# Performance work log

Hardware: AMD Instinct MI355X
Metric: run time of the kernel (lower is better)

## Reference

```python
import jax, jax.numpy as jnp
import numpy as np

B, T, D, S = 32, 4096, 64, 64
H = 128  # emission MLP hidden width
EPS = 1e-10
NEG = 1e10


def setup_inputs() -> dict:
    key = jax.random.key(0)
    ks = jax.random.split(key, 8)

    def dense_init(k, shape):
        return jax.random.normal(k, shape, jnp.float32) / jnp.sqrt(shape[0])

    return {
        "observations": jax.random.normal(ks[0], (B, T, D), jnp.float32),
        "W1": dense_init(ks[1], (D, H)), "b1": jnp.zeros((H,), jnp.float32),
        "W2": dense_init(ks[2], (H, H)), "b2": jnp.zeros((H,), jnp.float32),
        "W3": dense_init(ks[3], (H, S)), "b3": jnp.zeros((S,), jnp.float32),
        "log_trans_matrix": jax.random.normal(ks[4], (S, S), jnp.float32) * 0.1,
        "log_init_probs": jnp.zeros((S,), jnp.float32),
        "log_r": jnp.ones((S,), jnp.float32),
        "logit_p": jnp.zeros((S,), jnp.float32),
    }


def reference(observations, W1, b1, W2, b2, W3, b3,
              log_trans_matrix, log_init_probs, log_r, logit_p):
    # ---- emission MLP + softmax ----  (B,T,D) -> (B,T,S)
    h = jax.nn.relu(observations @ W1 + b1)
    h = jax.nn.relu(h @ W2 + b2)
    emission_probs = jax.nn.softmax(h @ W3 + b3, axis=-1)
    log_em = jnp.log(emission_probs + EPS)  # (B,T,S)

    # ---- transition probs: self-transition masked softmax (S,S) ----
    eye = jnp.eye(S, dtype=jnp.float32)
    masked_logits = log_trans_matrix * (1.0 - eye) - NEG * eye
    trans_probs = jax.nn.softmax(masked_logits, axis=-1)  # (S,S)
    log_trans = jnp.log(trans_probs + EPS)

    # ---- forward recursion (scan over time) ----
    # NOTE: t=0 uses log(emission) WITHOUT eps, matching the torch source.
    la0 = jax.nn.log_softmax(log_init_probs) + jnp.log(emission_probs[:, 0])  # (B,S)

    def fstep(la, le_t):  # la:(B,S), le_t:(B,S)
        la_t = jax.nn.logsumexp(la[:, :, None] + log_trans[None], axis=1) + le_t
        return la_t, la_t

    le_rest = jnp.swapaxes(log_em[:, 1:], 0, 1)  # (T-1,B,S)
    _, las = jax.lax.scan(fstep, la0, le_rest)
    log_alpha = jnp.concatenate([la0[:, None], jnp.swapaxes(las, 0, 1)], axis=1)  # (B,T,S)

    # ---- backward recursion ----
    lbT = jnp.zeros((B, S), jnp.float32)

    def bstep(lb, le_t1):  # combine emission(t+1)+beta(t+1) over next-state axis
        lb_t = jax.nn.logsumexp(log_trans[None] + (le_t1 + lb)[:, None, :], axis=2)
        return lb_t, lb_t

    _, lbs = jax.lax.scan(bstep, lbT, le_rest[::-1])  # lbs[0] is t=T-2
    log_beta = jnp.concatenate(
        [jnp.swapaxes(lbs, 0, 1)[:, ::-1], lbT[:, None]], axis=1)  # (B,T,S)

    # ---- posteriors ----
    log_gamma = log_alpha + log_beta
    log_gamma = log_gamma - jax.nn.logsumexp(log_gamma, axis=-1, keepdims=True)
    state_probs = jnp.exp(log_gamma)  # (B,T,S)
    state_marginals = state_probs.mean(axis=1)  # (B,S)

    # ---- expected durations (negative binomial) for all states ----
    r = jnp.exp(log_r)
    p = jax.nn.sigmoid(logit_p)
    expected_durations = r * (1.0 - p) / p  # (S,)

    # log-likelihood from final forward messages
    log_likelihood = jax.nn.logsumexp(log_alpha[:, -1], axis=-1)  # (B,)

    return state_probs, state_marginals, expected_durations, log_likelihood
```

## Files before the change

kernel.cpp:

```cpp
#include <hip/hip_runtime.h>

#define B_ 32
#define T_ 4096
#define D_ 64
#define H_ 128
#define S_ 64
#define BTS (B_*T_*S_)

#define NCH 512
#define CL  8
#define WU  12

#define EM_OFF    0
#define BETA_OFF  BTS
#define P_OFF     (2*BTS)
#define PT_OFF    (2*BTS + 4096)
#define INITP_OFF (2*BTS + 8192)
#define WSPLIT_OFF (BETA_OFF + BTS - 32768)
#define SP_OFF   0
#define MARG_OFF BTS
#define DUR_OFF  (BTS + 2048)
#define LL_OFF   (BTS + 2112)

typedef __attribute__((ext_vector_type(8))) short short8;
typedef __attribute__((ext_vector_type(4))) float f32x4;
#define MFMA_BF16 __builtin_amdgcn_mfma_f32_16x16x32_bf16

__device__ __forceinline__ float wsum(float v) {
    #pragma unroll
    for (int m = 1; m < 64; m <<= 1) v += __shfl_xor(v, m, 64);
    return v;
}
__device__ __forceinline__ float wmax(float v) {
    #pragma unroll
    for (int m = 1; m < 64; m <<= 1) v = fmaxf(v, __shfl_xor(v, m, 64));
    return v;
}
__device__ __forceinline__ unsigned short bfhi(float x) {
    return (unsigned short)(__float_as_uint(x) >> 16);
}
__device__ __forceinline__ float bf2f(unsigned short h) {
    return __uint_as_float(((unsigned int)h) << 16);
}
__device__ __forceinline__ void split8(const float* x8, short8& hi, short8& lo) {
    int hv[4], lv[4];
    #pragma unroll
    for (int p = 0; p < 4; p++) {
        float a = x8[2*p], b = x8[2*p+1];
        int h;
        asm("v_cvt_pk_bf16_f32 %0, %1, %2" : "=v"(h) : "v"(a), "v"(b));
        float ra = a - __uint_as_float(((unsigned)h) << 16);
        float rb = b - __uint_as_float(((unsigned)h) & 0xffff0000u);
        int l;
        asm("v_cvt_pk_bf16_f32 %0, %1, %2" : "=v"(l) : "v"(ra), "v"(rb));
        hv[p] = h; lv[p] = l;
    }
    hi = *(short8*)hv;
    lo = *(short8*)lv;
}

__global__ __launch_bounds__(256) void prep_k(const float* __restrict__ LT,
                                              const float* __restrict__ lip,
                                              const float* __restrict__ logr,
                                              const float* __restrict__ logitp,
                                              const float* __restrict__ W1,
                                              const float* __restrict__ W2,
                                              const float* __restrict__ W3,
                                              float* __restrict__ ws,
                                              float* __restrict__ out) {
    int tid = threadIdx.x, wid = tid >> 6, lane = tid & 63;
    if (blockIdx.x == 0) {
        for (int r = wid; r < S_; r += 4) {
            float x = (lane == r) ? -1e10f : LT[r * S_ + lane];
            float m = wmax(x);
            float e = __expf(x - m);
            float s = wsum(e);
            float p = e / s + 1e-10f;
            ws[P_OFF  + r * S_ + lane] = p;
            ws[PT_OFF + lane * S_ + r] = p;
        }
        if (wid == 0) {
            float x = lip[lane];
            float m = wmax(x);
            float e = __expf(x - m);
            float s = wsum(e);
            ws[INITP_OFF + lane] = e / s;
        } else if (wid == 1) {
            float r = __expf(logr[lane]);
            float p = 1.f / (1.f + __expf(-logitp[lane]));
            out[DUR_OFF + lane] = r * (1.f - p) / p;
        }
        for (int i = tid; i < B_ * S_; i += 256) out[MARG_OFF + i] = 0.f;
        if (tid < B_) out[LL_OFF + tid] = 0.f;
    }
    int gid = blockIdx.x * 256 + tid, gstr = gridDim.x * 256;
    unsigned short* wsp = (unsigned short*)(ws + WSPLIT_OFF);
    for (int i = gid; i < 8192; i += gstr) {
        int j = i >> 6, d = i & 63;
        float x = W1[d * 128 + j];
        unsigned short h = bfhi(x);
        wsp[i] = h;
        wsp[8192 + i] = bfhi(x - bf2f(h));
    }
    for (int i = gid; i < 16384; i += gstr) {
        int j = i >> 7, k = i & 127;
        float x = W2[k * 128 + j];
        unsigned short h = bfhi(x);
        wsp[16384 + i] = h;
        wsp[32768 + i] = bfhi(x - bf2f(h));
    }
    for (int i = gid; i < 8192; i += gstr) {
        int s = i >> 7, k = i & 127;
        float x = W3[k * 64 + s];
        unsigned short h = bfhi(x);
        wsp[49152 + i] = h;
        wsp[57344 + i] = bfhi(x - bf2f(h));
    }
}

__global__ __launch_bounds__(256) void mlp_k(const float* __restrict__ obs,
                                             const unsigned short* __restrict__ wsp,
                                             const float* __restrict__ b1,
                                             const float* __restrict__ b2,
                                             const float* __restrict__ b3,
                                             float* __restrict__ em) {
    __shared__ float lds[4 * 2112];
    int tid = threadIdx.x, wid = tid >> 6, lane = tid & 63;
    int c = lane & 15, q = lane >> 4;
    float* lb = lds + wid * 2112;
    int r0 = blockIdx.x * 128 + wid * 32;

    short8 a1h[2][2], a1l[2][2];
    #pragma unroll
    for (int mt = 0; mt < 2; mt++) {
        #pragma unroll
        for (int kq = 0; kq < 2; kq++) {
            const float* xp = obs + (size_t)(r0 + mt * 16 + c) * 64 + kq * 32 + q * 8;
            float x8[8];
            *(float4*)x8       = *(const float4*)xp;
            *(float4*)(x8 + 4) = *(const float4*)(xp + 4);
            split8(x8, a1h[mt][kq], a1l[mt][kq]);
        }
    }

    f32x4 D[2][8];
    #pragma unroll
    for (int nt = 0; nt < 8; nt++) {
        const unsigned short* wp = wsp + (nt * 16 + c) * 64 + q * 8;
        short8 bh0 = *(const short8*)(wp);
        short8 bh1 = *(const short8*)(wp + 32);
        short8 bl0 = *(const short8*)(wp + 8192);
        short8 bl1 = *(const short8*)(wp + 8192 + 32);
        #pragma unroll
        for (int mt = 0; mt < 2; mt++) {
            f32x4 acc = {0.f, 0.f, 0.f, 0.f};
            acc = MFMA_BF16(a1h[mt][0], bh0, acc, 0, 0, 0);
            acc = MFMA_BF16(a1h[mt][0], bl0, acc, 0, 0, 0);
            acc = MFMA_BF16(a1l[mt][0], bh0, acc, 0, 0, 0);
            acc = MFMA_BF16(a1h[mt][1], bh1, acc, 0, 0, 0);
            acc = MFMA_BF16(a1h[mt][1], bl1, acc, 0, 0, 0);
            acc = MFMA_BF16(a1l[mt][1], bh1, acc, 0, 0, 0);
            D[mt][nt] = acc;
        }
    }

    short8 a2h[2][4], a2l[2][4];
    #pragma unroll
    for (int mt = 0; mt < 2; mt++) {
        #pragma unroll
        for (int nt = 0; nt < 8; nt++) {
            float bb = b1[nt * 16 + c];
            f32x4 a = D[mt][nt];
            #pragma unroll
            for (int r = 0; r < 4; r++)
                lb[(q * 4 + r) * 132 + nt * 16 + c] = fmaxf(a[r] + bb, 0.f);
        }
        #pragma unroll
        for (int kq = 0; kq < 4; kq++) {
            float h8[8];
            *(float4*)h8       = *(const float4*)&lb[c * 132 + kq * 32 + q * 8];
            *(float4*)(h8 + 4) = *(const float4*)&lb[c * 132 + kq * 32 + q * 8 + 4];
            split8(h8, a2h[mt][kq], a2l[mt][kq]);
        }
        __asm__ __volatile__("s_waitcnt lgkmcnt(0)" ::: "memory");
    }

    #pragma unroll
    for (int nt = 0; nt < 8; nt++) {
        const unsigned short* wp = wsp + 16384 + (nt * 16 + c) * 128 + q * 8;
        short8 bh[4], bl[4];
        #pragma unroll
        for (int kq = 0; kq < 4; kq++) {
            bh[kq] = *(const short8*)(wp + kq * 32);
            bl[kq] = *(const short8*)(wp + 16384 + kq * 32);
        }
        #pragma unroll
        for (int mt = 0; mt < 2; mt++) {
            f32x4 acc = {0.f, 0.f, 0.f, 0.f};
            #pragma unroll
            for (int kq = 0; kq < 4; kq++) {
                acc = MFMA_BF16(a2h[mt][kq], bh[kq], acc, 0, 0, 0);
                acc = MFMA_BF16(a2h[mt][kq], bl[kq], acc, 0, 0, 0);
                acc = MFMA_BF16(a2l[mt][kq], bh[kq], acc, 0, 0, 0);
            }
            D[mt][nt] = acc;
        }
    }

    short8 a3h[2][4], a3l[2][4];
    #pragma unroll
    for (int mt = 0; mt < 2; mt++) {
        #pragma unroll
        for (int nt = 0; nt < 8; nt++) {
            float bb = b2[nt * 16 + c];
            f32x4 a = D[mt][nt];
            #pragma unroll
            for (int r = 0; r < 4; r++)
                lb[(q * 4 + r) * 132 + nt * 16 + c] = fmaxf(a[r] + bb, 0.f);
        }
        #pragma unroll
        for (int kq = 0; kq < 4; kq++) {
            float h8[8];
            *(float4*)h8       = *(const float4*)&lb[c * 132 + kq * 32 + q * 8];
            *(float4*)(h8 + 4) = *(const float4*)&lb[c * 132 + kq * 32 + q * 8 + 4];
            split8(h8, a3h[mt][kq], a3l[mt][kq]);
        }
        __asm__ __volatile__("s_waitcnt lgkmcnt(0)" ::: "memory");
    }

    f32x4 L[2][4];
    #pragma unroll
    for (int nt = 0; nt < 4; nt++) {
        const unsigned short* wp = wsp + 49152 + (nt * 16 + c) * 128 + q * 8;
        short8 bh[4], bl[4];
        #pragma unroll
        for (int kq = 0; kq < 4; kq++) {
            bh[kq] = *(const short8*)(wp + kq * 32);
            bl[kq] = *(const short8*)(wp + 8192 + kq * 32);
        }
        #pragma unroll
        for (int mt = 0; mt < 2; mt++) {
            f32x4 acc = {0.f, 0.f, 0.f, 0.f};
            #pragma unroll
            for (int kq = 0; kq < 4; kq++) {
                acc = MFMA_BF16(a3h[mt][kq], bh[kq], acc, 0, 0, 0);
                acc = MFMA_BF16(a3h[mt][kq], bl[kq], acc, 0, 0, 0);
                acc = MFMA_BF16(a3l[mt][kq], bh[kq], acc, 0, 0, 0);
            }
            L[mt][nt] = acc;
        }
    }

    float bb3[4];
    #pragma unroll
    for (int nt = 0; nt < 4; nt++) bb3[nt] = b3[nt * 16 + c];
    #pragma unroll
    for (int mt = 0; mt < 2; mt++) {
        #pragma unroll
        for (int r = 0; r < 4; r++) {
            float v[4];
            #pragma unroll
            for (int nt = 0; nt < 4; nt++) v[nt] = L[mt][nt][r] + bb3[nt];
            float m = fmaxf(fmaxf(v[0], v[1]), fmaxf(v[2], v[3]));
            #pragma unroll
            for (int msk = 1; msk < 16; msk <<= 1) m = fmaxf(m, __shfl_xor(m, msk, 64));
            float e[4], s = 0.f;
            #pragma unroll
            for (int nt = 0; nt < 4; nt++) { e[nt] = __expf(v[nt] - m); s += e[nt]; }
            #pragma unroll
            for (int msk = 1; msk < 16; msk <<= 1) s += __shfl_xor(s, msk, 64);
            float rs = __builtin_amdgcn_rcpf(s);
            size_t row = (size_t)(r0 + mt * 16 + q * 4 + r);
            #pragma unroll
            for (int nt = 0; nt < 4; nt++)
                em[row * 64 + nt * 16 + c] = e[nt] * rs;
        }
    }
}

__global__ __launch_bounds__(64) void scan_k(const float* __restrict__ em,
                                             const float* __restrict__ Pm,
                                             const float* __restrict__ PTm,
                                             const float* __restrict__ initp,
                                             float* __restrict__ alpha,
                                             float* __restrict__ beta,
                                             float* __restrict__ ll) {
    __shared__ float lds[16 * 68];
    const int lane = threadIdx.x, c = lane & 15, q = lane >> 4;
    int blk = blockIdx.x;
    const bool isf = blk < 2 * NCH;
    int lin = isf ? blk : blk - 2 * NCH;
    int bg = lin / NCH, ch = lin % NCH;
    const int b = bg * 16 + c;
    const float* M = isf ? PTm : Pm;

    short8 Bh[4][2], Bl[4][2];
    #pragma unroll
    for (int nt = 0; nt < 4; nt++) {
        #pragma unroll
        for (int kf = 0; kf < 2; kf++) {
            const float* mp = M + (nt * 16 + c) * 64 + kf * 32 + q * 8;
            float m8[8];
            *(float4*)m8       = *(const float4*)mp;
            *(float4*)(m8 + 4) = *(const float4*)(mp + 4);
            split8(m8, Bh[nt][kf], Bl[nt][kf]);
        }
    }

    const size_t ebase = (size_t)b * T_ * 64 + q * 8;
    float* outp = isf ? alpha : beta;
    const int wrofs = (q * 4) * 68 + c;
    const int rdofs = c * 68 + q * 8;

    float w[16];
    float rcpS, C = 0.f;

    auto loadE = [&](int t, float* e) {
        const float* p = em + ebase + (size_t)t * 64;
        *(float4*)(e)      = *(const float4*)(p);
        *(float4*)(e + 4)  = *(const float4*)(p + 4);
        *(float4*)(e + 8)  = *(const float4*)(p + 32);
        *(float4*)(e + 12) = *(const float4*)(p + 36);
    };
    auto storeY = [&](const float* y, int t) {
        float* p = outp + ebase + (size_t)t * 64;
        *(float4*)(p)      = *(const float4*)(y);
        *(float4*)(p + 4)  = *(const float4*)(y + 4);
        *(float4*)(p + 32) = *(const float4*)(y + 8);
        *(float4*)(p + 36) = *(const float4*)(y + 12);
    };
    auto chainsum = [&](const float* y) {
        float s = ((y[0]+y[1])+(y[2]+y[3])) + ((y[4]+y[5])+(y[6]+y[7]))
                + ((y[8]+y[9])+(y[10]+y[11])) + ((y[12]+y[13])+(y[14]+y[15]));
        s += __shfl_xor(s, 16, 64);
        s += __shfl_xor(s, 32, 64);
        return s;
    };
    auto matstep = [&](const float* z, float* y) {
        short8 ah0, al0, ah1, al1;
        split8(z, ah0, al0);
        split8(z + 8, ah1, al1);
        f32x4 Dv[4];
        #pragma unroll
        for (int nt = 0; nt < 4; nt++) {
            f32x4 acc = {0.f, 0.f, 0.f, 0.f};
            acc = MFMA_BF16(ah0, Bh[nt][0], acc, 0, 0, 0);
            acc = MFMA_BF16(al0, Bh[nt][0], acc, 0, 0, 0);
            acc = MFMA_BF16(ah0, Bl[nt][0], acc, 0, 0, 0);
            acc = MFMA_BF16(ah1, Bh[nt][1], acc, 0, 0, 0);
            acc = MFMA_BF16(al1, Bh[nt][1], acc, 0, 0, 0);
            acc = MFMA_BF16(ah1, Bl[nt][1], acc, 0, 0, 0);
            Dv[nt] = acc;
        }
        #pragma unroll
        for (int r = 0; r < 4; r++) {
            lds[wrofs + r * 68]      = Dv[0][r];
            lds[wrofs + r * 68 + 16] = Dv[1][r];
            lds[wrofs + r * 68 + 32] = Dv[2][r];
            lds[wrofs + r * 68 + 48] = Dv[3][r];
        }
        __asm__ __volatile__("s_waitcnt lgkmcnt(0)" ::: "memory");
        *(float4*)(y)      = *(const float4*)&lds[rdofs];
        *(float4*)(y + 4)  = *(const float4*)&lds[rdofs + 4];
        *(float4*)(y + 8)  = *(const float4*)&lds[rdofs + 32];
        *(float4*)(y + 12) = *(const float4*)&lds[rdofs + 36];
        __asm__ __volatile__("s_waitcnt lgkmcnt(0)" ::: "memory");
    };

    if (isf) {
        const int wlo = ch * CL, te = wlo + CL - 1;
        int ts, nwarm;
        if (ch == 0) {
            float e[16], ip[16];
            loadE(0, e);
            const float* pp = initp + q * 8;
            *(float4*)(ip)      = *(const float4*)(pp);
            *(float4*)(ip + 4)  = *(const float4*)(pp + 4);
            *(float4*)(ip + 8)  = *(const float4*)(pp + 32);
            *(float4*)(ip + 12) = *(const float4*)(pp + 36);
            #pragma unroll
            for (int i = 0; i < 16; i++) w[i] = ip[i] * e[i];
            storeY(w, 0);
            float s = chainsum(w);
            rcpS = __builtin_amdgcn_rcpf(s);
            C = __log2f(s);
            ts = 1; nwarm = 0;
        } else {
            ts = wlo - WU; if (ts < 1) ts = 1;
            nwarm = wlo - ts;
            float e[16];
            loadE(ts - 1, e);
            #pragma unroll
            for (int i = 0; i < 16; i++) w[i] = e[i] + 1e-10f;
            float s = chainsum(w);
            rcpS = __builtin_amdgcn_rcpf(s);
            C = 0.f;
        }
        auto stepF = [&](int t, bool owned) {
            float e[16];
            loadE(t, e);
            float y[16];
            matstep(w, y);
            float epsr = 1e-10f * rcpS;
            #pragma unroll
            for (int i = 0; i < 16; i++) y[i] *= fmaf(e[i], rcpS, epsr);
            float s = chainsum(y);
            if (owned) { C += __log2f(s); storeY(y, t); }
            rcpS = __builtin_amdgcn_rcpf(s);
            #pragma unroll
            for (int i = 0; i < 16; i++) w[i] = y[i];
        };
        for (int i = 0; i < nwarm; i++) stepF(ts + i, false);
        for (int t = wlo > 0 ? wlo : 1; t <= te; t++) stepF(t, true);
        if (q == 0) atomicAdd(&ll[b], C * 0.69314718056f);
    } else {
        const int tlo = ch * CL;
        const int whi = (ch == NCH - 1) ? T_ - 2 : tlo + CL - 1;
        int ts, nwarm;
        if (ch == NCH - 1) {
            float ones[16];
            #pragma unroll
            for (int i = 0; i < 16; i++) ones[i] = 1.f;
            storeY(ones, T_ - 1);
            float e[16];
            loadE(T_ - 1, e);
            #pragma unroll
            for (int i = 0; i < 16; i++) w[i] = e[i] + 1e-10f;
            rcpS = 1.f / 64.f;
            nwarm = 0; ts = T_ - 2;
        } else {
            ts = whi + WU; if (ts > T_ - 2) ts = T_ - 2;
            nwarm = ts - whi;
            float e[16];
            loadE(ts + 1, e);
            #pragma unroll
            for (int i = 0; i < 16; i++) w[i] = e[i] + 1e-10f;
            rcpS = 1.f / 64.f;
        }
        auto stepB = [&](int t, bool owned) {
            float e[16];
            loadE(t, e);
            float y[16];
            matstep(w, y);
            #pragma unroll
            for (int i = 0; i < 16; i++) y[i] *= rcpS;
            float s = chainsum(y);
            if (owned) storeY(y, t);
            rcpS = __builtin_amdgcn_rcpf(s);
            #pragma unroll
            for (int i = 0; i < 16; i++) w[i] = y[i] * (e[i] + 1e-10f);
        };
        for (int i = 0; i < nwarm; i++) stepB(ts - i, false);
        for (int t = whi; t >= tlo; t--) stepB(t, true);
    }
}

__global__ __launch_bounds__(256) void gamma_k(const float* __restrict__ beta,
                                               float* __restrict__ out) {
    int tid = threadIdx.x;
    int wid = tid >> 6, lane = tid & 63;
    int c = lane & 15, q = lane >> 4;
    int b = blockIdx.x >> 5;
    int tile = blockIdx.x & 31;
    int t0 = tile * 128 + wid * 32;
    float m0 = 0.f, m1 = 0.f, m2 = 0.f, m3 = 0.f;
    #pragma unroll
    for (int it = 0; it < 8; it++) {
        int row = t0 + it * 4 + q;
        size_t off = ((size_t)b * T_ + row) * 64 + c * 4;
        float4 a  = *(const float4*)&out[off];
        float4 be = *(const float4*)&beta[off];
        float px = a.x * be.x, py = a.y * be.y, pz = a.z * be.z, pw = a.w * be.w;
        float s = (px + py) + (pz + pw);
        s += __shfl_xor(s, 1, 64);
        s += __shfl_xor(s, 2, 64);
        s += __shfl_xor(s, 4, 64);
        s += __shfl_xor(s, 8, 64);
        float rs = __builtin_amdgcn_rcpf(fmaxf(s, 1e-37f));
        float4 g;
        g.x = px * rs; g.y = py * rs; g.z = pz * rs; g.w = pw * rs;
        *(float4*)&out[off] = g;
        m0 += g.x; m1 += g.y; m2 += g.z; m3 += g.w;
    }
    m0 += __shfl_xor(m0, 16, 64); m0 += __shfl_xor(m0, 32, 64);
    m1 += __shfl_xor(m1, 16, 64); m1 += __shfl_xor(m1, 32, 64);
    m2 += __shfl_xor(m2, 16, 64); m2 += __shfl_xor(m2, 32, 64);
    m3 += __shfl_xor(m3, 16, 64); m3 += __shfl_xor(m3, 32, 64);
    if (q == 0) {
        const float sc = 1.0f / T_;
        atomicAdd(&out[MARG_OFF + b * 64 + 4 * c + 0], m0 * sc);
        atomicAdd(&out[MARG_OFF + b * 64 + 4 * c + 1], m1 * sc);
        atomicAdd(&out[MARG_OFF + b * 64 + 4 * c + 2], m2 * sc);
        atomicAdd(&out[MARG_OFF + b * 64 + 4 * c + 3], m3 * sc);
    }
}

extern "C" void kernel_launch(void* const* d_in, const int* in_sizes, int n_in,
                              void* d_out, int out_size, void* d_ws, size_t ws_size,
                              hipStream_t stream) {
    (void)in_sizes; (void)n_in; (void)out_size; (void)ws_size;
    const float* obs    = (const float*)d_in[0];
    const float* W1     = (const float*)d_in[1];
    const float* b1     = (const float*)d_in[2];
    const float* W2     = (const float*)d_in[3];
    const float* b2     = (const float*)d_in[4];
    const float* W3     = (const float*)d_in[5];
    const float* b3     = (const float*)d_in[6];
    const float* LT     = (const float*)d_in[7];
    const float* lip    = (const float*)d_in[8];
    const float* logr   = (const float*)d_in[9];
    const float* logitp = (const float*)d_in[10];
    float* out = (float*)d_out;
    float* ws  = (float*)d_ws;

    hipLaunchKernelGGL(prep_k, dim3(64), dim3(256), 0, stream,
                       LT, lip, logr, logitp, W1, W2, W3, ws, out);
    hipLaunchKernelGGL(mlp_k, dim3(1024), dim3(256), 0, stream,
                       obs, (const unsigned short*)(ws + WSPLIT_OFF),
                       b1, b2, b3, ws + EM_OFF);
    hipLaunchKernelGGL(scan_k, dim3(4 * NCH), dim3(64), 0, stream,
                       ws + EM_OFF, ws + P_OFF, ws + PT_OFF, ws + INITP_OFF,
                       out + SP_OFF, ws + BETA_OFF, out + LL_OFF);
    hipLaunchKernelGGL(gamma_k, dim3(1024), dim3(256), 0, stream, ws + BETA_OFF, out);
}
```

Measured before the change: 246.1 us.

## Split scan into forward and backward kernels; fuse posterior normalization into backward

The combined forward/backward scan kernel becomes two kernels. The backward kernel now reads alpha and normalizes the posterior in place, which removes the separate gamma pass and the beta round-trip through memory. Per-chunk marginal partials are written to workspace and reduced by a small kernel instead of using atomics. The cost is that the forward and backward scans, which used to run concurrently in one grid, are now serialized, which may leave the GPU underused during each half.

```diff
diff --git a/kernel.cpp b/kernel.cpp
--- a/kernel.cpp
+++ b/kernel.cpp
@@ -90,7 +90,6 @@
             float p = 1.f / (1.f + __expf(-logitp[lane]));
             out[DUR_OFF + lane] = r * (1.f - p) / p;
         }
-        for (int i = tid; i < B_ * S_; i += 256) out[MARG_OFF + i] = 0.f;
         if (tid < B_) out[LL_OFF + tid] = 0.f;
     }
     int gid = blockIdx.x * 256 + tid, gstr = gridDim.x * 256;
@@ -278,21 +277,17 @@
     }
 }
 
-__global__ __launch_bounds__(64) void scan_k(const float* __restrict__ em,
-                                             const float* __restrict__ Pm,
-                                             const float* __restrict__ PTm,
-                                             const float* __restrict__ initp,
-                                             float* __restrict__ alpha,
-                                             float* __restrict__ beta,
-                                             float* __restrict__ ll) {
+__global__ __launch_bounds__(64) void scan_fwd_k(const float* __restrict__ em,
+                                                 const float* __restrict__ PTm,
+                                                 const float* __restrict__ initp,
+                                                 float* __restrict__ alpha,
+                                                 float* __restrict__ ll) {
     __shared__ float lds[16 * 68];
     const int lane = threadIdx.x, c = lane & 15, q = lane >> 4;
-    int blk = blockIdx.x;
-    const bool isf = blk < 2 * NCH;
-    int lin = isf ? blk : blk - 2 * NCH;
+    int lin = blockIdx.x;
     int bg = lin / NCH, ch = lin % NCH;
     const int b = bg * 16 + c;
-    const float* M = isf ? PTm : Pm;
+    const float* M = PTm;
 
     short8 Bh[4][2], Bl[4][2];
     #pragma unroll
@@ -308,10 +303,8 @@
     }
 
     const size_t ebase = (size_t)b * T_ * 64 + q * 8;
-    float* outp = isf ? alpha : beta;
     const int wrofs = (q * 4) * 68 + c;
     const int rdofs = c * 68 + q * 8;
-
     float w[16];
     float rcpS, C = 0.f;
 
@@ -323,7 +316,7 @@
         *(float4*)(e + 12) = *(const float4*)(p + 36);
     };
     auto storeY = [&](const float* y, int t) {
-        float* p = outp + ebase + (size_t)t * 64;
+        float* p = alpha + ebase + (size_t)t * 64;
         *(float4*)(p)      = *(const float4*)(y);
         *(float4*)(p + 4)  = *(const float4*)(y + 4);
         *(float4*)(p + 32) = *(const float4*)(y + 8);
@@ -367,132 +360,217 @@
         __asm__ __volatile__("s_waitcnt lgkmcnt(0)" ::: "memory");
     };
 
-    if (isf) {
-        const int wlo = ch * CL, te = wlo + CL - 1;
-        int ts, nwarm;
-        if (ch == 0) {
-            float e[16], ip[16];
-            loadE(0, e);
-            const float* pp = initp + q * 8;
-            *(float4*)(ip)      = *(const float4*)(pp);
-            *(float4*)(ip + 4)  = *(const float4*)(pp + 4);
-            *(float4*)(ip + 8)  = *(const float4*)(pp + 32);
-            *(float4*)(ip + 12) = *(const float4*)(pp + 36);
-            #pragma unroll
-            for (int i = 0; i < 16; i++) w[i] = ip[i] * e[i];
-            storeY(w, 0);
-            float s = chainsum(w);
-            rcpS = __builtin_amdgcn_rcpf(s);
-            C = __log2f(s);
-            ts = 1; nwarm = 0;
-        } else {
-            ts = wlo - WU; if (ts < 1) ts = 1;
-            nwarm = wlo - ts;
-            float e[16];
-            loadE(ts - 1, e);
-            #pragma unroll
-            for (int i = 0; i < 16; i++) w[i] = e[i] + 1e-10f;
-            float s = chainsum(w);
-            rcpS = __builtin_amdgcn_rcpf(s);
-            C = 0.f;
-        }
-        auto stepF = [&](int t, bool owned) {
-            float e[16];
-            loadE(t, e);
-            float y[16];
-            matstep(w, y);
-            float epsr = 1e-10f * rcpS;
-            #pragma unroll
-            for (int i = 0; i < 16; i++) y[i] *= fmaf(e[i], rcpS, epsr);
-            float s = chainsum(y);
-            if (owned) { C += __log2f(s); storeY(y, t); }
-            rcpS = __builtin_amdgcn_rcpf(s);
-            #pragma unroll
-            for (int i = 0; i < 16; i++) w[i] = y[i];
-        };
-        for (int i = 0; i < nwarm; i++) stepF(ts + i, false);
-        for (int t = wlo > 0 ? wlo : 1; t <= te; t++) stepF(t, true);
-        if (q == 0) atomicAdd(&ll[b], C * 0.69314718056f);
+    const int wlo = ch * CL, te = wlo + CL - 1;
+    int ts, nwarm;
+    if (ch == 0) {
+        float e[16], ip[16];
+        loadE(0, e);
+        const float* pp = initp + q * 8;
+        *(float4*)(ip)      = *(const float4*)(pp);
+        *(float4*)(ip + 4)  = *(const float4*)(pp + 4);
+        *(float4*)(ip + 8)  = *(const float4*)(pp + 32);
+        *(float4*)(ip + 12) = *(const float4*)(pp + 36);
+        #pragma unroll
+        for (int i = 0; i < 16; i++) w[i] = ip[i] * e[i];
+        storeY(w, 0);
+        float s = chainsum(w);
+        rcpS = __builtin_amdgcn_rcpf(s);
+        C = __log2f(s);
+        ts = 1; nwarm = 0;
     } else {
-        const int tlo = ch * CL;
-        const int whi = (ch == NCH - 1) ? T_ - 2 : tlo + CL - 1;
-        int ts, nwarm;
-        if (ch == NCH - 1) {
-            float ones[16];
-            #pragma unroll
-            for (int i = 0; i < 16; i++) ones[i] = 1.f;
-            storeY(ones, T_ - 1);
-            float e[16];
-            loadE(T_ - 1, e);
-            #pragma unroll
-            for (int i = 0; i < 16; i++) w[i] = e[i] + 1e-10f;
-            rcpS = 1.f / 64.f;
-            nwarm = 0; ts = T_ - 2;
-        } else {
-            ts = whi + WU; if (ts > T_ - 2) ts = T_ - 2;
-            nwarm = ts - whi;
-            float e[16];
-            loadE(ts + 1, e);
-            #pragma unroll
-            for (int i = 0; i < 16; i++) w[i] = e[i] + 1e-10f;
-            rcpS = 1.f / 64.f;
-        }
-        auto stepB = [&](int t, bool owned) {
-            float e[16];
-            loadE(t, e);
-            float y[16];
-            matstep(w, y);
-            #pragma unroll
-            for (int i = 0; i < 16; i++) y[i] *= rcpS;
-            float s = chainsum(y);
-            if (owned) storeY(y, t);
-            rcpS = __builtin_amdgcn_rcpf(s);
-            #pragma unroll
-            for (int i = 0; i < 16; i++) w[i] = y[i] * (e[i] + 1e-10f);
-        };
-        for (int i = 0; i < nwarm; i++) stepB(ts - i, false);
-        for (int t = whi; t >= tlo; t--) stepB(t, true);
-    }
-}
-
-__global__ __launch_bounds__(256) void gamma_k(const float* __restrict__ beta,
-                                               float* __restrict__ out) {
-    int tid = threadIdx.x;
-    int wid = tid >> 6, lane = tid & 63;
-    int c = lane & 15, q = lane >> 4;
-    int b = blockIdx.x >> 5;
-    int tile = blockIdx.x & 31;
-    int t0 = tile * 128 + wid * 32;
-    float m0 = 0.f, m1 = 0.f, m2 = 0.f, m3 = 0.f;
-    #pragma unroll
-    for (int it = 0; it < 8; it++) {
-        int row = t0 + it * 4 + q;
-        size_t off = ((size_t)b * T_ + row) * 64 + c * 4;
-        float4 a  = *(const float4*)&out[off];
-        float4 be = *(const float4*)&beta[off];
-        float px = a.x * be.x, py = a.y * be.y, pz = a.z * be.z, pw = a.w * be.w;
-        float s = (px + py) + (pz + pw);
-        s += __shfl_xor(s, 1, 64);
-        s += __shfl_xor(s, 2, 64);
-        s += __shfl_xor(s, 4, 64);
-        s += __shfl_xor(s, 8, 64);
-        float rs = __builtin_amdgcn_rcpf(fmaxf(s, 1e-37f));
-        float4 g;
-        g.x = px * rs; g.y = py * rs; g.z = pz * rs; g.w = pw * rs;
-        *(float4*)&out[off] = g;
-        m0 += g.x; m1 += g.y; m2 += g.z; m3 += g.w;
-    }
-    m0 += __shfl_xor(m0, 16, 64); m0 += __shfl_xor(m0, 32, 64);
-    m1 += __shfl_xor(m1, 16, 64); m1 += __shfl_xor(m1, 32, 64);
-    m2 += __shfl_xor(m2, 16, 64); m2 += __shfl_xor(m2, 32, 64);
-    m3 += __shfl_xor(m3, 16, 64); m3 += __shfl_xor(m3, 32, 64);
-    if (q == 0) {
-        const float sc = 1.0f / T_;
-        atomicAdd(&out[MARG_OFF + b * 64 + 4 * c + 0], m0 * sc);
-        atomicAdd(&out[MARG_OFF + b * 64 + 4 * c + 1], m1 * sc);
-        atomicAdd(&out[MARG_OFF + b * 64 + 4 * c + 2], m2 * sc);
-        atomicAdd(&out[MARG_OFF + b * 64 + 4 * c + 3], m3 * sc);
-    }
+        ts = wlo - WU; if (ts < 1) ts = 1;
+        nwarm = wlo - ts;
+        float e[16];
+        loadE(ts - 1, e);
+        #pragma unroll
+        for (int i = 0; i < 16; i++) w[i] = e[i] + 1e-10f;
+        float s = chainsum(w);
+        rcpS = __builtin_amdgcn_rcpf(s);
+        C = 0.f;
+    }
+    auto stepF = [&](int t, bool owned) {
+        float e[16];
+        loadE(t, e);
+        float y[16];
+        matstep(w, y);
+        float epsr = 1e-10f * rcpS;
+        #pragma unroll
+        for (int i = 0; i < 16; i++) y[i] *= fmaf(e[i], rcpS, epsr);
+        float s = chainsum(y);
+        if (owned) { C += __log2f(s); storeY(y, t); }
+        rcpS = __builtin_amdgcn_rcpf(s);
+        #pragma unroll
+        for (int i = 0; i < 16; i++) w[i] = y[i];
+    };
+    for (int i = 0; i < nwarm; i++) stepF(ts + i, false);
+    for (int t = wlo > 0 ? wlo : 1; t <= te; t++) stepF(t, true);
+    if (q == 0) atomicAdd(&ll[b], C * 0.69314718056f);
+}
+
+__global__ __launch_bounds__(64) void scan_bwd_k(const float* __restrict__ em,
+                                                 const float* __restrict__ Pm,
+                                                 float* __restrict__ gam,
+                                                 float* __restrict__ part) {
+    __shared__ float lds[16 * 68];
+    const int lane = threadIdx.x, c = lane & 15, q = lane >> 4;
+    int lin = blockIdx.x;
+    int bg = lin / NCH, ch = lin % NCH;
+    const int b = bg * 16 + c;
+    const float* M = Pm;
+
+    short8 Bh[4][2], Bl[4][2];
+    #pragma unroll
+    for (int nt = 0; nt < 4; nt++) {
+        #pragma unroll
+        for (int kf = 0; kf < 2; kf++) {
+            const float* mp = M + (nt * 16 + c) * 64 + kf * 32 + q * 8;
+            float m8[8];
+            *(float4*)m8       = *(const float4*)mp;
+            *(float4*)(m8 + 4) = *(const float4*)(mp + 4);
+            split8(m8, Bh[nt][kf], Bl[nt][kf]);
+        }
+    }
+
+    const size_t ebase = (size_t)b * T_ * 64 + q * 8;
+    const int wrofs = (q * 4) * 68 + c;
+    const int rdofs = c * 68 + q * 8;
+    float w[16];
+    float rcpS;
+    float macc[16];
+    #pragma unroll
+    for (int i = 0; i < 16; i++) macc[i] = 0.f;
+
+    auto loadE = [&](int t, float* e) {
+        const float* p = em + ebase + (size_t)t * 64;
+        *(float4*)(e)      = *(const float4*)(p);
+        *(float4*)(e + 4)  = *(const float4*)(p + 4);
+        *(float4*)(e + 8)  = *(const float4*)(p + 32);
+        *(float4*)(e + 12) = *(const float4*)(p + 36);
+    };
+    auto loadA = [&](int t, float* a) {
+        const float* p = gam + ebase + (size_t)t * 64;
+        *(float4*)(a)      = *(const float4*)(p);
+        *(float4*)(a + 4)  = *(const float4*)(p + 4);
+        *(float4*)(a + 8)  = *(const float4*)(p + 32);
+        *(float4*)(a + 12) = *(const float4*)(p + 36);
+    };
+    auto storeG = [&](const float* y, int t) {
+        float* p = gam + ebase + (size_t)t * 64;
+        *(float4*)(p)      = *(const float4*)(y);
+        *(float4*)(p + 4)  = *(const float4*)(y + 4);
+        *(float4*)(p + 32) = *(const float4*)(y + 8);
+        *(float4*)(p + 36) = *(const float4*)(y + 12);
+    };
+    auto chainsum = [&](const float* y) {
+        float s = ((y[0]+y[1])+(y[2]+y[3])) + ((y[4]+y[5])+(y[6]+y[7]))
+                + ((y[8]+y[9])+(y[10]+y[11])) + ((y[12]+y[13])+(y[14]+y[15]));
+        s += __shfl_xor(s, 16, 64);
+        s += __shfl_xor(s, 32, 64);
+        return s;
+    };
+    auto matstep = [&](const float* z, float* y) {
+        short8 ah0, al0, ah1, al1;
+        split8(z, ah0, al0);
+        split8(z + 8, ah1, al1);
+        f32x4 Dv[4];
+        #pragma unroll
+        for (int nt = 0; nt < 4; nt++) {
+            f32x4 acc = {0.f, 0.f, 0.f, 0.f};
+            acc = MFMA_BF16(ah0, Bh[nt][0], acc, 0, 0, 0);
+            acc = MFMA_BF16(al0, Bh[nt][0], acc, 0, 0, 0);
+            acc = MFMA_BF16(ah0, Bl[nt][0], acc, 0, 0, 0);
+            acc = MFMA_BF16(ah1, Bh[nt][1], acc, 0, 0, 0);
+            acc = MFMA_BF16(al1, Bh[nt][1], acc, 0, 0, 0);
+            acc = MFMA_BF16(ah1, Bl[nt][1], acc, 0, 0, 0);
+            Dv[nt] = acc;
+        }
+        #pragma unroll
+        for (int r = 0; r < 4; r++) {
+            lds[wrofs + r * 68]      = Dv[0][r];
+            lds[wrofs + r * 68 + 16] = Dv[1][r];
+            lds[wrofs + r * 68 + 32] = Dv[2][r];
+            lds[wrofs + r * 68 + 48] = Dv[3][r];
+        }
+        __asm__ __volatile__("s_waitcnt lgkmcnt(0)" ::: "memory");
+        *(float4*)(y)      = *(const float4*)&lds[rdofs];
+        *(float4*)(y + 4)  = *(const float4*)&lds[rdofs + 4];
+        *(float4*)(y + 8)  = *(const float4*)&lds[rdofs + 32];
+        *(float4*)(y + 12) = *(const float4*)&lds[rdofs + 36];
+        __asm__ __volatile__("s_waitcnt lgkmcnt(0)" ::: "memory");
+    };
+
+    const int tlo = ch * CL;
+    const int whi = (ch == NCH - 1) ? T_ - 2 : tlo + CL - 1;
+    int ts, nwarm;
+    if (ch == NCH - 1) {
+        float a[16];
+        loadA(T_ - 1, a);
+        float ps = chainsum(a);
+        float rg = __builtin_amdgcn_rcpf(fmaxf(ps, 1e-37f));
+        #pragma unroll
+        for (int i = 0; i < 16; i++) { a[i] *= rg; macc[i] += a[i]; }
+        storeG(a, T_ - 1);
+        float e[16];
+        loadE(T_ - 1, e);
+        #pragma unroll
+        for (int i = 0; i < 16; i++) w[i] = e[i] + 1e-10f;
+        rcpS = 1.f / 64.f;
+        nwarm = 0; ts = T_ - 2;
+    } else {
+        ts = whi + WU; if (ts > T_ - 2) ts = T_ - 2;
+        nwarm = ts - whi;
+        float e[16];
+        loadE(ts + 1, e);
+        #pragma unroll
+        for (int i = 0; i < 16; i++) w[i] = e[i] + 1e-10f;
+        rcpS = 1.f / 64.f;
+    }
+    auto stepB = [&](int t, bool owned) {
+        float e[16];
+        loadE(t, e);
+        float a[16];
+        if (owned) loadA(t, a);
+        float y[16];
+        matstep(w, y);
+        #pragma unroll
+        for (int i = 0; i < 16; i++) y[i] *= rcpS;
+        float s = chainsum(y);
+        if (owned) {
+            float p[16];
+            #pragma unroll
+            for (int i = 0; i < 16; i++) p[i] = a[i] * y[i];
+            float ps = chainsum(p);
+            float rg = __builtin_amdgcn_rcpf(fmaxf(ps, 1e-37f));
+            #pragma unroll
+            for (int i = 0; i < 16; i++) { p[i] *= rg; macc[i] += p[i]; }
+            storeG(p, t);
+        }
+        rcpS = __builtin_amdgcn_rcpf(s);
+        #pragma unroll
+        for (int i = 0; i < 16; i++) w[i] = y[i] * (e[i] + 1e-10f);
+    };
+    for (int i = 0; i < nwarm; i++) stepB(ts - i, false);
+    for (int t = whi; t >= tlo; t--) stepB(t, true);
+
+    float* pp = part + (size_t)lin * 1024 + lane * 16;
+    *(float4*)(pp)      = *(const float4*)(macc);
+    *(float4*)(pp + 4)  = *(const float4*)(macc + 4);
+    *(float4*)(pp + 8)  = *(const float4*)(macc + 8);
+    *(float4*)(pp + 12) = *(const float4*)(macc + 12);
+}
+
+__global__ __launch_bounds__(256) void marg_k(const float* __restrict__ part,
+                                              float* __restrict__ out) {
+    int gid = blockIdx.x * 256 + threadIdx.x;
+    int b = gid >> 6, s = gid & 63;
+    int c = b & 15, bg = b >> 4;
+    int q = (s & 31) >> 3;
+    int i = (s < 32) ? (s & 7) : 8 + (s & 7);
+    int idx = (q * 16 + c) * 16 + i;
+    const float* p = part + (size_t)bg * NCH * 1024 + idx;
+    float acc = 0.f;
+    for (int ch = 0; ch < NCH; ch++) acc += p[(size_t)ch * 1024];
+    out[MARG_OFF + b * 64 + s] = acc * (1.0f / T_);
 }
 
 extern "C" void kernel_launch(void* const* d_in, const int* in_sizes, int n_in,
@@ -518,8 +596,11 @@
     hipLaunchKernelGGL(mlp_k, dim3(1024), dim3(256), 0, stream,
                        obs, (const unsigned short*)(ws + WSPLIT_OFF),
                        b1, b2, b3, ws + EM_OFF);
-    hipLaunchKernelGGL(scan_k, dim3(4 * NCH), dim3(64), 0, stream,
-                       ws + EM_OFF, ws + P_OFF, ws + PT_OFF, ws + INITP_OFF,
-                       out + SP_OFF, ws + BETA_OFF, out + LL_OFF);
-    hipLaunchKernelGGL(gamma_k, dim3(1024), dim3(256), 0, stream, ws + BETA_OFF, out);
-}
+    hipLaunchKernelGGL(scan_fwd_k, dim3(2 * NCH), dim3(64), 0, stream,
+                       ws + EM_OFF, ws + PT_OFF, ws + INITP_OFF,
+                       out + SP_OFF, out + LL_OFF);
+    hipLaunchKernelGGL(scan_bwd_k, dim3(2 * NCH), dim3(64), 0, stream,
+                       ws + EM_OFF, ws + P_OFF, out + SP_OFF, ws + BETA_OFF);
+    hipLaunchKernelGGL(marg_k, dim3(8), dim3(256), 0, stream,
+                       ws + BETA_OFF, out);
+}
```

Result: slower. 260.7 us (+5.9%).
